# Kernel optimization log

Hardware: AMD Instinct MI355X
Metric: run time of the kernel (lower is better)

## Reference

```python
import jax, jax.numpy as jnp
import numpy as np


def _conv3x3(x, w, b):
    # x: [B,C,H,W], w: [O,C,3,3], b: [O]; stride 1, padding 1 (SAME)
    y = jax.lax.conv_general_dilated(
        x, w,
        window_strides=(1, 1),
        padding=((1, 1), (1, 1)),
        dimension_numbers=("NCHW", "OIHW", "NCHW"),
    )
    return y + b[None, :, None, None]


def setup_inputs() -> dict:
    key = jax.random.key(0)
    k_x, k_w1, k_b1, k_w2, k_b2 = jax.random.split(key, 5)
    B, Cin, H, W = 16, 128, 96, 96
    Ch = 256
    # Kaiming-ish small init for conv weights
    x = jax.random.normal(k_x, (B, Cin, H, W), dtype=jnp.float32)
    w1 = jax.random.normal(k_w1, (Ch, Cin, 3, 3), dtype=jnp.float32) * (1.0 / np.sqrt(Cin * 9))
    b1 = jax.random.normal(k_b1, (Ch,), dtype=jnp.float32) * 0.01
    w2 = jax.random.normal(k_w2, (2, Ch, 3, 3), dtype=jnp.float32) * (1.0 / np.sqrt(Ch * 9))
    b2 = jax.random.normal(k_b2, (2,), dtype=jnp.float32) * 0.01
    return {"x": x, "w1": w1, "b1": b1, "w2": w2, "b2": b2}


def reference(x, w1, b1, w2, b2):
    # DeformConv2d with zero offsets == plain 3x3 conv (stride 1, pad 1) + bias.
    h = jax.nn.relu(_conv3x3(x, w1, b1))  # [B,256,H,W]
    return _conv3x3(h, w2, b2)            # [B,2,H,W]
```

## Files before the change

kernel.cpp:

```cpp
#include <hip/hip_runtime.h>
#include <stdint.h>

typedef unsigned short ushort_t;
typedef __attribute__((ext_vector_type(8))) short short8;
typedef __attribute__((ext_vector_type(4))) float floatx4;
typedef __attribute__((ext_vector_type(4))) unsigned short ushortx4;
typedef __attribute__((ext_vector_type(8))) unsigned short ushortx8;

#define B_   16
#define CIN  128
#define CH   256
#define HW   96
#define HP   98

#define XPAD_ELEMS (B_*HP*HP*CIN)
#define HPAD_ELEMS (B_*HP*HP*CH)
#define XPAD_OFF 0
#define HPAD_OFF (XPAD_ELEMS*2)
#define W1T_OFF  (HPAD_OFF + HPAD_ELEMS*2)
#define W2T_OFF  (W1T_OFF + 256*1152*2)

__device__ __forceinline__ ushort_t f2bf(float f){
  uint32_t u = __float_as_uint(f);
  u += 0x7FFF + ((u >> 16) & 1);
  return (ushort_t)(u >> 16);
}
__device__ __forceinline__ float bf2f(ushort_t h){
  return __uint_as_float(((uint32_t)h) << 16);
}
__device__ __forceinline__ void async_ld16(void* lds, const void* g){
  __builtin_amdgcn_global_load_lds(
      (const __attribute__((address_space(1))) void*)g,
      (__attribute__((address_space(3))) void*)lds, 16, 0, 0);
}

__device__ __forceinline__ void zb(uint32_t* base, int C2, int tid){
  int perimg = 388*C2;
  int b = tid / perimg; int r = tid % perimg;
  int cell = r / C2;    int cu = r % C2;
  int y, x;
  if      (cell < 98)  { y = 0;            x = cell;       }
  else if (cell < 196) { y = 97;           x = cell - 98;  }
  else if (cell < 292) { y = cell - 195;   x = 0;          }
  else                 { y = cell - 291;   x = 97;         }
  base[((b*HP + y)*HP + x)*C2 + cu] = 0u;
}

__global__ __launch_bounds__(256) void prep_all(const float* __restrict__ x,
                                                const float* __restrict__ w1,
                                                const float* __restrict__ w2,
                                                uint32_t* __restrict__ xpadw,
                                                uint32_t* __restrict__ hpadw,
                                                ushort_t* __restrict__ w1t,
                                                float* __restrict__ w2t,
                                                ushort_t* __restrict__ xpad){
  __shared__ float lds[128][33];
  int bidx = blockIdx.x;
  int t = threadIdx.x;
  if (bidx < 4608){
    int xt = bidx % 3; int y = (bidx/3) % 96; int b = bidx/288;
    int x0 = xt*32;
    #pragma unroll
    for (int rep=0; rep<16; ++rep){
      int idx = rep*256 + t;
      int ci = idx >> 5, xj = idx & 31;
      lds[ci][xj] = x[((b*CIN + ci)*HW + y)*HW + x0 + xj];
    }
    __syncthreads();
    int px = t & 31, oc = t >> 5;
    ushort_t* dst = &xpad[((b*HP + y+1)*HP + x0+px+1)*CIN + oc*16];
    ushortx8 v0, v1;
    #pragma unroll
    for (int k=0;k<8;k++) v0[k] = f2bf(lds[oc*16+k][px]);
    #pragma unroll
    for (int k=0;k<8;k++) v1[k] = f2bf(lds[oc*16+8+k][px]);
    *(ushortx8*)dst = v0;
    *(ushortx8*)(dst+8) = v1;
  } else {
    int tid = (bidx - 4608)*256 + t;
    const int NZX = B_*388*64;
    const int NZH = B_*388*128;
    const int NW1 = 256*1152;
    if (tid < NZX){
      zb(xpadw, 64, tid);
    } else if (tid < NZX + NZH){
      zb(hpadw, 128, tid - NZX);
    } else if (tid < NZX + NZH + NW1){
      int r = tid - (NZX + NZH);
      int o = r / 1152, k = r - o*1152;
      int tap = k >> 7, c = k & 127;
      w1t[r] = f2bf(w1[(o*CIN + c)*9 + tap]);
    } else {
      int r = tid - (NZX + NZH + NW1);
      int ch = r & 1, c = (r >> 1) & 255, tap = r >> 9;
      w2t[r] = w2[(ch*CH + c)*9 + tap];
    }
  }
}

#define C1_TILE(KT, VMN, SA, SB) { \
  asm volatile("s_waitcnt vmcnt(" #VMN ")" ::: "memory"); \
  __builtin_amdgcn_s_barrier(); \
  __builtin_amdgcn_sched_barrier(0); \
  const int kt_ = (KT); \
  const ushort_t* Ab = &Alds[(kt_ & 1) * 8192]; \
  const ushort_t* Bb = &Blds[(kt_ % 3) * 8192]; \
  short8 a0[4], a1[4], b0[2], b1[2], b2v[2], b3[2]; \
   \
  _Pragma("unroll") \
  for (int nf=0; nf<2; ++nf) b0[nf] = *(const short8*)&Bb[bbase_r + nf*1024 + koff0]; \
  _Pragma("unroll") \
  for (int mf=0; mf<4; ++mf) a0[mf] = *(const short8*)&Ab[abase_r + mf*1024 + koff0]; \
  if (SA) { \
    const int ka_ = kt_ + 1; const int ab_ = (ka_ & 1) * 8192; \
    async_ld16(&Alds[ab_ +    0 + adst], &w1t[asrc +       0 + ka_*64]); \
    async_ld16(&Alds[ab_ + 2048 + adst], &w1t[asrc +   36864 + ka_*64]); \
  } \
  __builtin_amdgcn_s_barrier(); \
  asm volatile("s_waitcnt lgkmcnt(0)" ::: "memory"); \
  __builtin_amdgcn_sched_barrier(0); \
  __builtin_amdgcn_s_setprio(1); \
  _Pragma("unroll") \
  for (int mf=0; mf<4; ++mf) \
    _Pragma("unroll") \
    for (int nf=0; nf<2; ++nf) \
      acc[mf][nf] = __builtin_amdgcn_mfma_f32_16x16x32_bf16(a0[mf], b0[nf], acc[mf][nf], 0,0,0); \
  __builtin_amdgcn_s_setprio(0); \
  __builtin_amdgcn_s_barrier(); \
  __builtin_amdgcn_sched_barrier(0); \
   \
  _Pragma("unroll") \
  for (int nf=0; nf<2; ++nf) b1[nf] = *(const short8*)&Bb[bbase_r + (nf+2)*1024 + koff0]; \
  if (SA) { \
    const int ka_ = kt_ + 1; const int ab_ = (ka_ & 1) * 8192; \
    async_ld16(&Alds[ab_ + 4096 + adst], &w1t[asrc + 2*36864 + ka_*64]); \
    async_ld16(&Alds[ab_ + 6144 + adst], &w1t[asrc + 3*36864 + ka_*64]); \
  } \
  __builtin_amdgcn_s_barrier(); \
  asm volatile("s_waitcnt lgkmcnt(0)" ::: "memory"); \
  __builtin_amdgcn_sched_barrier(0); \
  __builtin_amdgcn_s_setprio(1); \
  _Pragma("unroll") \
  for (int mf=0; mf<4; ++mf) \
    _Pragma("unroll") \
    for (int nf=0; nf<2; ++nf) \
      acc[mf][nf+2] = __builtin_amdgcn_mfma_f32_16x16x32_bf16(a0[mf], b1[nf], acc[mf][nf+2], 0,0,0); \
  __builtin_amdgcn_s_setprio(0); \
  __builtin_amdgcn_s_barrier(); \
  __builtin_amdgcn_sched_barrier(0); \
   \
  _Pragma("unroll") \
  for (int nf=0; nf<2; ++nf) b2v[nf] = *(const short8*)&Bb[bbase_r + nf*1024 + koff1]; \
  _Pragma("unroll") \
  for (int mf=0; mf<4; ++mf) a1[mf] = *(const short8*)&Ab[abase_r + mf*1024 + koff1]; \
  if (SB) { \
    const int kb_ = kt_ + 2; \
    const int tapb_ = kb_ >> 1; \
    const int dyb_ = tapb_/3; const int dxb_ = tapb_ - dyb_*3; \
    const int bdb_ = (dyb_*HP + dxb_)*CIN + (kb_&1)*64; \
    const int bb_ = (kb_ % 3) * 8192; \
    async_ld16(&Blds[bb_ +    0 + bdst], &xpad[bsrc +            bdb_]); \
    async_ld16(&Blds[bb_ + 2048 + bdst], &xpad[bsrc +   HP*CIN + bdb_]); \
  } \
  __builtin_amdgcn_s_barrier(); \
  asm volatile("s_waitcnt lgkmcnt(0)" ::: "memory"); \
  __builtin_amdgcn_sched_barrier(0); \
  __builtin_amdgcn_s_setprio(1); \
  _Pragma("unroll") \
  for (int mf=0; mf<4; ++mf) \
    _Pragma("unroll") \
    for (int nf=0; nf<2; ++nf) \
      acc[mf][nf] = __builtin_amdgcn_mfma_f32_16x16x32_bf16(a1[mf], b2v[nf], acc[mf][nf], 0,0,0); \
  __builtin_amdgcn_s_setprio(0); \
  __builtin_amdgcn_s_barrier(); \
  __builtin_amdgcn_sched_barrier(0); \
   \
  _Pragma("unroll") \
  for (int nf=0; nf<2; ++nf) b3[nf] = *(const short8*)&Bb[bbase_r + (nf+2)*1024 + koff1]; \
  if (SB) { \
    const int kb_ = kt_ + 2; \
    const int tapb_ = kb_ >> 1; \
    const int dyb_ = tapb_/3; const int dxb_ = tapb_ - dyb_*3; \
    const int bdb_ = (dyb_*HP + dxb_)*CIN + (kb_&1)*64; \
    const int bb_ = (kb_ % 3) * 8192; \
    async_ld16(&Blds[bb_ + 4096 + bdst], &xpad[bsrc + 2*HP*CIN + bdb_]); \
    async_ld16(&Blds[bb_ + 6144 + bdst], &xpad[bsrc + 3*HP*CIN + bdb_]); \
  } \
  __builtin_amdgcn_s_barrier(); \
  asm volatile("s_waitcnt lgkmcnt(0)" ::: "memory"); \
  __builtin_amdgcn_sched_barrier(0); \
  __builtin_amdgcn_s_setprio(1); \
  _Pragma("unroll") \
  for (int mf=0; mf<4; ++mf) \
    _Pragma("unroll") \
    for (int nf=0; nf<2; ++nf) \
      acc[mf][nf+2] = __builtin_amdgcn_mfma_f32_16x16x32_bf16(a1[mf], b3[nf], acc[mf][nf+2], 0,0,0); \
  __builtin_amdgcn_s_setprio(0); \
}

__global__ __launch_bounds__(256, 2) void conv1(const ushort_t* __restrict__ xpad,
                                                const ushort_t* __restrict__ w1t,
                                                const float* __restrict__ b1,
                                                ushort_t* __restrict__ hpad){
  __shared__ __align__(16) ushort_t Alds[2*8192];
  __shared__ __align__(16) ushort_t Blds[3*8192];
  int orig = blockIdx.x;
  int bid = (orig & 7) * 288 + (orig >> 3);
  int mt = bid & 1;
  int nt = bid >> 1;
  int b = nt / 72; int rem = nt - b*72;
  int y0 = (rem/3)*4, x0 = (rem - (rem/3)*3)*32;
  int o0 = mt*128;
  int t = threadIdx.x;
  int lane = t & 63, wave = t >> 6;
  int wm = wave & 1, wn = wave >> 1;
  int r = lane & 15, q = lane >> 4;

  const int arow0 = t >> 3;
  const int soct  = (t & 7) ^ (arow0 & 7);
  const int adst  = t * 8;
  const int asrc  = (o0 + arow0) * 1152 + soct * 8;
  const int bdst  = t * 8;
  const int bsrc  = ((b*HP + y0)*HP + x0 + arow0)*CIN + soct * 8;

  const int koff0 = ((0*4 + q) ^ (r & 7)) * 8;
  const int koff1 = ((1*4 + q) ^ (r & 7)) * 8;
  const int abase_r = (wm*64 + r) * 64;
  const int bbase_r = (wn*64 + r) * 64;

  floatx4 acc[4][4];
  #pragma unroll
  for (int i=0;i<4;i++)
    #pragma unroll
    for (int j=0;j<4;j++) acc[i][j] = (floatx4){0.f,0.f,0.f,0.f};

  #pragma unroll
  for (int j=0;j<4;++j) async_ld16(&Blds[0    + j*2048 + bdst], &xpad[bsrc + j*HP*CIN]);
  #pragma unroll
  for (int j=0;j<4;++j) async_ld16(&Alds[0    + j*2048 + adst], &w1t[asrc + j*36864]);
  #pragma unroll
  for (int j=0;j<4;++j) async_ld16(&Blds[8192 + j*2048 + bdst], &xpad[bsrc + j*HP*CIN + 64]);

  for (int kt=0; kt<16; ++kt){
    C1_TILE(kt, 4, 1, 1)
  }
  C1_TILE(16, 4, 1, 0)
  C1_TILE(17, 0, 0, 0)

  #pragma unroll
  for (int mf=0; mf<4; ++mf){
    int o = o0 + wm*64 + mf*16 + q*4;
    float bias0 = b1[o], bias1 = b1[o+1], bias2 = b1[o+2], bias3 = b1[o+3];
    #pragma unroll
    for (int nf=0; nf<4; ++nf){
      int n = wn*64 + nf*16 + r;
      int ty = n >> 5, tx = n & 31;
      ushortx4 v;
      v[0] = f2bf(fmaxf(acc[mf][nf][0] + bias0, 0.f));
      v[1] = f2bf(fmaxf(acc[mf][nf][1] + bias1, 0.f));
      v[2] = f2bf(fmaxf(acc[mf][nf][2] + bias2, 0.f));
      v[3] = f2bf(fmaxf(acc[mf][nf][3] + bias3, 0.f));
      *(ushortx4*)&hpad[((b*HP + y0+ty+1)*HP + (x0+tx+1))*CH + o] = v;
    }
  }
}

__global__ __launch_bounds__(256) void conv2(const ushort_t* __restrict__ hpad,
                                             const float* __restrict__ w2t,
                                             const float* __restrict__ b2,
                                             float* __restrict__ out){
  __shared__ __align__(16) ushort_t hlds[25600];
  __shared__ float part[4][64][2];
  int bid = blockIdx.x;
  int b = bid / 144; int rem = bid - b*144;
  int yt = rem / 12, xt = rem - yt*12;
  int y0 = yt*8, x0 = xt*8;
  int t = threadIdx.x;
  int wave = t >> 6, lane = t & 63;

  for (int pass=0; pass<13; ++pass){
    int u = pass*256 + t;
    if (u < 3200){
      int cell = u >> 5, cf = u & 31;
      int hy = cell / 10, hx = cell - hy*10;
      const ushort_t* src = hpad + ((b*HP + y0+hy)*HP + (x0+hx))*CH
                                 + ((cf ^ (cell & 7)) << 3);
      async_ld16(&hlds[(pass*256 + wave*64)*8], src);
    }
  }
  __syncthreads();

  int q = __builtin_amdgcn_readfirstlane(wave);
  int ty = lane >> 3, tx = lane & 7;
  float a0 = 0.f, a1 = 0.f;
  for (int tap=0; tap<9; ++tap){
    int dy = tap/3, dxx = tap - dy*3;
    int cell = (ty+dy)*10 + (tx+dxx);
    int s = cell & 7;
    const float* wp = w2t + (tap*256 + q*64)*2;
    #pragma unroll
    for (int g=0; g<8; ++g){
      int j = q*8 + g;
      ushortx8 hv = *(const ushortx8*)&hlds[cell*256 + ((j ^ s) << 3)];
      #pragma unroll
      for (int i=0;i<8;i++){
        float hf = bf2f(hv[i]);
        a0 = fmaf(hf, wp[(g*8+i)*2    ], a0);
        a1 = fmaf(hf, wp[(g*8+i)*2 + 1], a1);
      }
    }
  }
  part[wave][lane][0] = a0;
  part[wave][lane][1] = a1;
  __syncthreads();
  if (t < 128){
    int sel = t >> 6, pix = t & 63;
    float v = part[0][pix][sel] + part[1][pix][sel]
            + part[2][pix][sel] + part[3][pix][sel] + b2[sel];
    int yy = y0 + (pix >> 3), xx = x0 + (pix & 7);
    out[(b*2 + sel)*9216 + yy*96 + xx] = v;
  }
}

extern "C" void kernel_launch(void* const* d_in, const int* in_sizes, int n_in,
                              void* d_out, int out_size, void* d_ws, size_t ws_size,
                              hipStream_t stream){
  const float* x  = (const float*)d_in[0];
  const float* w1 = (const float*)d_in[1];
  const float* b1 = (const float*)d_in[2];
  const float* w2 = (const float*)d_in[3];
  const float* b2 = (const float*)d_in[4];
  float* out = (float*)d_out;
  char* ws = (char*)d_ws;
  ushort_t* xpad = (ushort_t*)(ws + XPAD_OFF);
  ushort_t* hpad = (ushort_t*)(ws + HPAD_OFF);
  ushort_t* w1t  = (ushort_t*)(ws + W1T_OFF);
  float*    w2t  = (float*)(ws + W2T_OFF);

  hipLaunchKernelGGL(prep_all, dim3(10434), dim3(256), 0, stream,
                     x, w1, w2, (uint32_t*)xpad, (uint32_t*)hpad, w1t, w2t, xpad);
  hipLaunchKernelGGL(conv1, dim3(2304), dim3(256), 0, stream, xpad, w1t, b1, hpad);
  hipLaunchKernelGGL(conv2, dim3(2304), dim3(256), 0, stream, hpad, w2t, b2, out);
}
```

Baseline: 164.0 us.

## Load conv1 activation fragments directly from global memory, dropping B LDS staging

The conv1 kernel stops staging the input-activation (B) tiles in a triple-buffered LDS ring and instead loads each lane's MFMA B fragments straight from the padded NHWC bf16 input in global memory. Only the weights still go through LDS, which shrinks shared memory use and raises the launch-bounds occupancy hint from 2 to 3 blocks per CU. The prep kernel also processes four rows per block, cutting its grid size. In exchange, the B loads are now synchronous global loads with vmcnt(0) waits each k-tile and are no longer prefetched. This risks exposing memory latency and relies on L1/L2 caching for reuse across the 3x3 taps.

```diff
diff --git a/kernel.cpp b/kernel.cpp
--- a/kernel.cpp
+++ b/kernel.cpp
@@ -57,27 +57,31 @@
   __shared__ float lds[128][33];
   int bidx = blockIdx.x;
   int t = threadIdx.x;
-  if (bidx < 4608){
-    int xt = bidx % 3; int y = (bidx/3) % 96; int b = bidx/288;
-    int x0 = xt*32;
-    #pragma unroll
-    for (int rep=0; rep<16; ++rep){
-      int idx = rep*256 + t;
-      int ci = idx >> 5, xj = idx & 31;
-      lds[ci][xj] = x[((b*CIN + ci)*HW + y)*HW + x0 + xj];
-    }
-    __syncthreads();
-    int px = t & 31, oc = t >> 5;
-    ushort_t* dst = &xpad[((b*HP + y+1)*HP + x0+px+1)*CIN + oc*16];
-    ushortx8 v0, v1;
-    #pragma unroll
-    for (int k=0;k<8;k++) v0[k] = f2bf(lds[oc*16+k][px]);
-    #pragma unroll
-    for (int k=0;k<8;k++) v1[k] = f2bf(lds[oc*16+8+k][px]);
-    *(ushortx8*)dst = v0;
-    *(ushortx8*)(dst+8) = v1;
+  if (bidx < 1152){
+    int xt = bidx % 3; int yt = (bidx/3) % 24; int b = bidx/72;
+    int x0 = xt*32, y0 = yt*4;
+    for (int yy=0; yy<4; ++yy){
+      int y = y0 + yy;
+      #pragma unroll
+      for (int rep=0; rep<16; ++rep){
+        int idx = rep*256 + t;
+        int ci = idx >> 5, xj = idx & 31;
+        lds[ci][xj] = x[((b*CIN + ci)*HW + y)*HW + x0 + xj];
+      }
+      __syncthreads();
+      int px = t & 31, oc = t >> 5;
+      ushort_t* dst = &xpad[((b*HP + y+1)*HP + x0+px+1)*CIN + oc*16];
+      ushortx8 v0, v1;
+      #pragma unroll
+      for (int k=0;k<8;k++) v0[k] = f2bf(lds[oc*16+k][px]);
+      #pragma unroll
+      for (int k=0;k<8;k++) v1[k] = f2bf(lds[oc*16+8+k][px]);
+      *(ushortx8*)dst = v0;
+      *(ushortx8*)(dst+8) = v1;
+      __syncthreads();
+    }
   } else {
-    int tid = (bidx - 4608)*256 + t;
+    int tid = (bidx - 1152)*256 + t;
     const int NZX = B_*388*64;
     const int NZH = B_*388*128;
     const int NW1 = 256*1152;
@@ -98,17 +102,21 @@
   }
 }
 
-#define C1_TILE(KT, VMN, SA, SB) { \
-  asm volatile("s_waitcnt vmcnt(" #VMN ")" ::: "memory"); \
+#define C1_TILE(KT, SA) { \
+  asm volatile("s_waitcnt vmcnt(0)" ::: "memory"); \
   __builtin_amdgcn_s_barrier(); \
   __builtin_amdgcn_sched_barrier(0); \
   const int kt_ = (KT); \
   const ushort_t* Ab = &Alds[(kt_ & 1) * 8192]; \
-  const ushort_t* Bb = &Blds[(kt_ % 3) * 8192]; \
+  const int tap_ = kt_ >> 1; \
+  const int dy_ = tap_/3; const int dx_ = tap_ - dy_*3; \
+  const int bd_ = (dy_*HP + dx_)*CIN + (kt_&1)*64; \
   short8 a0[4], a1[4], b0[2], b1[2], b2v[2], b3[2]; \
    \
-  _Pragma("unroll") \
-  for (int nf=0; nf<2; ++nf) b0[nf] = *(const short8*)&Bb[bbase_r + nf*1024 + koff0]; \
+  b0[0] = *(const short8*)&xpad[bgoff[0] + bd_]; \
+  b0[1] = *(const short8*)&xpad[bgoff[1] + bd_]; \
+  b1[0] = *(const short8*)&xpad[bgoff[2] + bd_]; \
+  b1[1] = *(const short8*)&xpad[bgoff[3] + bd_]; \
   _Pragma("unroll") \
   for (int mf=0; mf<4; ++mf) a0[mf] = *(const short8*)&Ab[abase_r + mf*1024 + koff0]; \
   if (SA) { \
@@ -129,8 +137,6 @@
   __builtin_amdgcn_s_barrier(); \
   __builtin_amdgcn_sched_barrier(0); \
    \
-  _Pragma("unroll") \
-  for (int nf=0; nf<2; ++nf) b1[nf] = *(const short8*)&Bb[bbase_r + (nf+2)*1024 + koff0]; \
   if (SA) { \
     const int ka_ = kt_ + 1; const int ab_ = (ka_ & 1) * 8192; \
     async_ld16(&Alds[ab_ + 4096 + adst], &w1t[asrc + 2*36864 + ka_*64]); \
@@ -149,19 +155,12 @@
   __builtin_amdgcn_s_barrier(); \
   __builtin_amdgcn_sched_barrier(0); \
    \
-  _Pragma("unroll") \
-  for (int nf=0; nf<2; ++nf) b2v[nf] = *(const short8*)&Bb[bbase_r + nf*1024 + koff1]; \
+  b2v[0] = *(const short8*)&xpad[bgoff[0] + bd_ + 32]; \
+  b2v[1] = *(const short8*)&xpad[bgoff[1] + bd_ + 32]; \
+  b3[0]  = *(const short8*)&xpad[bgoff[2] + bd_ + 32]; \
+  b3[1]  = *(const short8*)&xpad[bgoff[3] + bd_ + 32]; \
   _Pragma("unroll") \
   for (int mf=0; mf<4; ++mf) a1[mf] = *(const short8*)&Ab[abase_r + mf*1024 + koff1]; \
-  if (SB) { \
-    const int kb_ = kt_ + 2; \
-    const int tapb_ = kb_ >> 1; \
-    const int dyb_ = tapb_/3; const int dxb_ = tapb_ - dyb_*3; \
-    const int bdb_ = (dyb_*HP + dxb_)*CIN + (kb_&1)*64; \
-    const int bb_ = (kb_ % 3) * 8192; \
-    async_ld16(&Blds[bb_ +    0 + bdst], &xpad[bsrc +            bdb_]); \
-    async_ld16(&Blds[bb_ + 2048 + bdst], &xpad[bsrc +   HP*CIN + bdb_]); \
-  } \
   __builtin_amdgcn_s_barrier(); \
   asm volatile("s_waitcnt lgkmcnt(0)" ::: "memory"); \
   __builtin_amdgcn_sched_barrier(0); \
@@ -175,19 +174,7 @@
   __builtin_amdgcn_s_barrier(); \
   __builtin_amdgcn_sched_barrier(0); \
    \
-  _Pragma("unroll") \
-  for (int nf=0; nf<2; ++nf) b3[nf] = *(const short8*)&Bb[bbase_r + (nf+2)*1024 + koff1]; \
-  if (SB) { \
-    const int kb_ = kt_ + 2; \
-    const int tapb_ = kb_ >> 1; \
-    const int dyb_ = tapb_/3; const int dxb_ = tapb_ - dyb_*3; \
-    const int bdb_ = (dyb_*HP + dxb_)*CIN + (kb_&1)*64; \
-    const int bb_ = (kb_ % 3) * 8192; \
-    async_ld16(&Blds[bb_ + 4096 + bdst], &xpad[bsrc + 2*HP*CIN + bdb_]); \
-    async_ld16(&Blds[bb_ + 6144 + bdst], &xpad[bsrc + 3*HP*CIN + bdb_]); \
-  } \
-  __builtin_amdgcn_s_barrier(); \
-  asm volatile("s_waitcnt lgkmcnt(0)" ::: "memory"); \
+  __builtin_amdgcn_s_barrier(); \
   __builtin_amdgcn_sched_barrier(0); \
   __builtin_amdgcn_s_setprio(1); \
   _Pragma("unroll") \
@@ -198,12 +185,11 @@
   __builtin_amdgcn_s_setprio(0); \
 }
 
-__global__ __launch_bounds__(256, 2) void conv1(const ushort_t* __restrict__ xpad,
+__global__ __launch_bounds__(256, 3) void conv1(const ushort_t* __restrict__ xpad,
                                                 const ushort_t* __restrict__ w1t,
                                                 const float* __restrict__ b1,
                                                 ushort_t* __restrict__ hpad){
   __shared__ __align__(16) ushort_t Alds[2*8192];
-  __shared__ __align__(16) ushort_t Blds[3*8192];
   int orig = blockIdx.x;
   int bid = (orig & 7) * 288 + (orig >> 3);
   int mt = bid & 1;
@@ -220,13 +206,18 @@
   const int soct  = (t & 7) ^ (arow0 & 7);
   const int adst  = t * 8;
   const int asrc  = (o0 + arow0) * 1152 + soct * 8;
-  const int bdst  = t * 8;
-  const int bsrc  = ((b*HP + y0)*HP + x0 + arow0)*CIN + soct * 8;
 
   const int koff0 = ((0*4 + q) ^ (r & 7)) * 8;
   const int koff1 = ((1*4 + q) ^ (r & 7)) * 8;
   const int abase_r = (wm*64 + r) * 64;
-  const int bbase_r = (wn*64 + r) * 64;
+
+  int bgoff[4];
+  #pragma unroll
+  for (int nf=0; nf<4; ++nf){
+    int n = wn*64 + nf*16 + r;
+    int ty = n >> 5, tx = n & 31;
+    bgoff[nf] = ((b*HP + y0+ty)*HP + (x0+tx))*CIN + q*8;
+  }
 
   floatx4 acc[4][4];
   #pragma unroll
@@ -235,17 +226,12 @@
     for (int j=0;j<4;j++) acc[i][j] = (floatx4){0.f,0.f,0.f,0.f};
 
   #pragma unroll
-  for (int j=0;j<4;++j) async_ld16(&Blds[0    + j*2048 + bdst], &xpad[bsrc + j*HP*CIN]);
-  #pragma unroll
-  for (int j=0;j<4;++j) async_ld16(&Alds[0    + j*2048 + adst], &w1t[asrc + j*36864]);
-  #pragma unroll
-  for (int j=0;j<4;++j) async_ld16(&Blds[8192 + j*2048 + bdst], &xpad[bsrc + j*HP*CIN + 64]);
-
-  for (int kt=0; kt<16; ++kt){
-    C1_TILE(kt, 4, 1, 1)
-  }
-  C1_TILE(16, 4, 1, 0)
-  C1_TILE(17, 0, 0, 0)
+  for (int j=0;j<4;++j) async_ld16(&Alds[j*2048 + adst], &w1t[asrc + j*36864]);
+
+  for (int kt=0; kt<17; ++kt){
+    C1_TILE(kt, 1)
+  }
+  C1_TILE(17, 0)
 
   #pragma unroll
   for (int mf=0; mf<4; ++mf){
@@ -337,7 +323,7 @@
   ushort_t* w1t  = (ushort_t*)(ws + W1T_OFF);
   float*    w2t  = (float*)(ws + W2T_OFF);
 
-  hipLaunchKernelGGL(prep_all, dim3(10434), dim3(256), 0, stream,
+  hipLaunchKernelGGL(prep_all, dim3(6978), dim3(256), 0, stream,
                      x, w1, w2, (uint32_t*)xpad, (uint32_t*)hpad, w1t, w2t, xpad);
   hipLaunchKernelGGL(conv1, dim3(2304), dim3(256), 0, stream, xpad, w1t, b1, hpad);
   hipLaunchKernelGGL(conv2, dim3(2304), dim3(256), 0, stream, hpad, w2t, b2, out);
```

After: 241.3 us. 1.47x slower.
